# Kernel optimization log

Hardware: AMD Instinct MI355X
Metric: run time of the kernel (lower is better)

The kernel has to match this reference:

```python
import jax, jax.numpy as jnp
import numpy as np

SESSION_CHANNELS = [128, 160, 192, 224, 240, 248, 252, 256]  # per-session channel counts
N_SESS = len(SESSION_CHANNELS)
B, MAX_C, MAX_T = 16, 256, 4096
HID, N_SRC = 512, 256


def setup_inputs() -> dict:
    key = jax.random.key(0)
    ks = jax.random.split(key, 7)
    session_ids = jax.random.randint(ks[0], (B,), 0, N_SESS)
    chan_table = jnp.asarray(SESSION_CHANNELS)
    channel_counts = chan_table[session_ids]
    seq_lens = jax.random.randint(ks[1], (B,), MAX_T // 2, MAX_T + 1)
    x = jax.random.normal(ks[2], (B, MAX_C, MAX_T), jnp.float32)
    # zero-pad beyond true channels and true time (as the docstring states)
    cmask = (jnp.arange(MAX_C)[None, :] < channel_counts[:, None]).astype(x.dtype)
    tmask = (jnp.arange(MAX_T)[None, :] < seq_lens[:, None]).astype(x.dtype)
    x = x * cmask[:, :, None] * tmask[:, None, :]
    # per-session Linear(num_channels -> HID), padded to MAX_C rows (torch-style uniform init)
    lim1 = 1.0 / np.sqrt(MAX_C)
    W_sess = jax.random.uniform(ks[3], (N_SESS, MAX_C, HID), jnp.float32, -lim1, lim1)
    b_sess = jax.random.uniform(ks[4], (N_SESS, HID), jnp.float32, -lim1, lim1)
    lim2 = 1.0 / np.sqrt(HID)
    W2 = jax.random.uniform(ks[5], (HID, N_SRC), jnp.float32, -lim2, lim2)
    b2 = jax.random.uniform(ks[6], (N_SRC,), jnp.float32, -lim2, lim2)
    return dict(x=x, session_ids=session_ids, channel_counts=channel_counts,
                seq_lens=seq_lens, W_sess=W_sess, b_sess=b_sess, W2=W2, b2=b2)


def reference(x, session_ids, channel_counts, seq_lens, W_sess, b_sess, W2, b2):
    # mask padded channels so the full-width contraction equals the sliced per-sample matmul
    cmask = (jnp.arange(x.shape[1])[None, :] < channel_counts[:, None]).astype(x.dtype)
    xm = x * cmask[:, :, None]                       # (B, Max_C, Max_T)
    W = W_sess[session_ids]                          # (B, Max_C, HID) gathered per sample
    b = b_sess[session_ids]                          # (B, HID)
    h = jnp.einsum('bct,bch->bht', xm, W) + b[:, :, None]
    h = jax.nn.gelu(h, approximate=False)            # torch nn.GELU default is exact erf
    out = jnp.einsum('bht,hs->bst', h, W2) + b2[None, :, None]  # (B, N_SRC, Max_T)
    tmask = (jnp.arange(x.shape[2])[None, :] < seq_lens[:, None]).astype(x.dtype)
    return out * tmask[:, None, :]
```

## Files before the change

kernel.cpp:

```cpp
#include <hip/hip_runtime.h>

typedef __attribute__((ext_vector_type(8))) _Float16 f16x8;
typedef __attribute__((ext_vector_type(4))) _Float16 f16x4;
typedef __attribute__((ext_vector_type(2))) __fp16 fp16v2;
typedef __attribute__((ext_vector_type(4))) float f32x4;

#define NB 16
#define MAXC 256
#define MAXT 4096
#define HID 512
#define NSRC 256

#define BARV() asm volatile("s_waitcnt vmcnt(0) lgkmcnt(0)\n\ts_barrier" ::: "memory")
#define BAR() asm volatile("s_waitcnt lgkmcnt(0)\n\ts_barrier" ::: "memory")

#define MFMA(a, b, c) __builtin_amdgcn_mfma_f32_16x16x32_f16(a, b, c, 0, 0, 0)

typedef __attribute__((address_space(1))) const void gconst_void;
typedef __attribute__((address_space(3))) void lds_void;
#define GLOAD16(gp, lp) \
  __builtin_amdgcn_global_load_lds((gconst_void*)(gp), (lds_void*)(lp), 16, 0, 0)

__device__ __forceinline__ float gelu_fast(float x) {
  float p = x * x;
  float q = __builtin_fmaf(p, -0.10294336f, -2.30220778f);
  float e = __builtin_amdgcn_exp2f(x * q);
  return x * __builtin_amdgcn_rcpf(1.0f + e);
}

__device__ __forceinline__ void transpose_cvt_tile(const float* src, _Float16* dst,
                                                   int R, int C, int cx, int ry,
                                                   int tid) {
  __shared__ float tile[32][33];
  int c0 = cx * 32, r0 = ry * 32;
  int tx = tid & 31, ty = tid >> 5;
  for (int i = ty; i < 32; i += 8)
    tile[i][tx] = src[(size_t)(r0 + i) * C + (c0 + tx)];
  __syncthreads();
  for (int i = ty; i < 32; i += 8)
    dst[(size_t)(c0 + i) * R + (r0 + tx)] = (_Float16)tile[tx][i];
}

__global__ __launch_bounds__(256)
void prep_kernel(const float* __restrict__ x,
                 const int* __restrict__ seq_lens,
                 const int* __restrict__ chan_counts,
                 const float* __restrict__ W_sess,
                 const float* __restrict__ W2,
                 _Float16* __restrict__ xT,
                 _Float16* __restrict__ W1t,
                 _Float16* __restrict__ W2t) {
  int wg = blockIdx.x;
  int tid = threadIdx.x;

  if (wg >= 4096) {
    if (wg >= 5120) {
      int idx = wg - 5120;
      transpose_cvt_tile(W2, W2t, HID, NSRC, idx & 7, idx >> 3, tid);
    } else {
      int idx = wg - 4096;
      int z = idx >> 7;
      transpose_cvt_tile(W_sess + (size_t)z * MAXC * HID,
                         W1t + (size_t)z * MAXC * HID,
                         MAXC, HID, idx & 15, (idx >> 4) & 7, tid);
    }
    return;
  }

  int b = wg >> 8;
  int t0 = (wg & 63) * 64;
  int c0 = ((wg >> 6) & 3) * 64;
  int seqlen = seq_lens[b];
  if (t0 >= ((seqlen + 127) & ~127)) return;
  int wt = tid >> 5;
  int c2 = (tid & 31) * 2;
  _Float16* op = xT + ((size_t)b * MAXT + t0) * MAXC + c0;

  if (c0 >= chan_counts[b]) {
    #pragma unroll
    for (int i = 0; i < 8; ++i) {
      fp16v2 z = {(_Float16)0.f, (_Float16)0.f};
      *(fp16v2*)(op + (size_t)(wt + i * 8) * MAXC + c2) = z;
    }
    return;
  }

  __shared__ float tile[64][65];
  int tx = tid & 63, ty = tid >> 6;
  const float* xp = x + ((size_t)b * MAXC + c0) * MAXT + t0;
  #pragma unroll
  for (int i = 0; i < 16; ++i) {
    int c = ty + i * 4;
    tile[c][tx] = xp[(size_t)c * MAXT + tx];
  }
  __syncthreads();
  #pragma unroll
  for (int i = 0; i < 8; ++i) {
    int tl = wt + i * 8;
    fp16v2 p = __builtin_amdgcn_cvt_pkrtz(tile[c2][tl], tile[c2 + 1][tl]);
    *(fp16v2*)(op + (size_t)tl * MAXC + c2) = p;
  }
}


__global__ __launch_bounds__(512, 2)
void gemm1_kernel(const _Float16* __restrict__ xT,
                  const int* __restrict__ sess_ids,
                  const int* __restrict__ seq_lens,
                  const _Float16* __restrict__ W1t,
                  const float* __restrict__ b_sess,
                  _Float16* __restrict__ h_t) {
  int wg = blockIdx.x;
  int nt = wg & 31;
  int mt = (wg >> 5) & 1;
  int b = wg >> 6;
  int tb0 = nt * 128, h0 = mt * 256;
  int seqlen = seq_lens[b];
  if (tb0 >= seqlen) return;
  int sid = sess_ids[b];

  __shared__ _Float16 As[256 * 64];
  __shared__ _Float16 Bs[128 * 64];

  int tid = threadIdx.x;
  int lane = tid & 63, w = tid >> 6;
  int wr = w >> 1, wc = w & 1;
  int lg = lane >> 4, lr = lane & 15;

  f32x4 acc[4][4];
  #pragma unroll
  for (int mi = 0; mi < 4; ++mi) {
    f32x4 bv = *(const f32x4*)(b_sess + sid * HID + h0 + wr * 64 + mi * 16 + lg * 4);
    #pragma unroll
    for (int ni = 0; ni < 4; ++ni) acc[mi][ni] = bv;
  }

  int rsub = lane >> 3;
  int swb = ((lane & 7) ^ rsub) * 16;
  const char* gA = (const char*)(W1t + (size_t)sid * HID * MAXC + (size_t)h0 * MAXC)
                   + (size_t)(w * 32 + rsub) * 512 + swb;
  const char* gB = (const char*)(xT + ((size_t)b * MAXT + tb0) * MAXC)
                   + (size_t)(w * 16 + rsub) * 512 + swb;
  char* lA = (char*)As + w * 4096;
  char* lB = (char*)Bs + w * 2048;

#define STAGE1(kc)                                                        \
  {                                                                       \
    _Pragma("unroll")                                                     \
    for (int j = 0; j < 4; ++j)                                           \
      GLOAD16(gA + (size_t)(kc)*128 + (size_t)j * 8 * 512, lA + j * 1024); \
    _Pragma("unroll")                                                     \
    for (int j = 0; j < 2; ++j)                                           \
      GLOAD16(gB + (size_t)(kc)*128 + (size_t)j * 8 * 512, lB + j * 1024); \
  }

  STAGE1(0);
  BARV();

  #pragma unroll 1
  for (int kc = 0; kc < 4; ++kc) {
    #pragma unroll
    for (int slot = 0; slot < 2; ++slot) {
      f16x8 af[4], bf[4];
      #pragma unroll
      for (int mi = 0; mi < 4; ++mi) {
        int row = wr * 64 + mi * 16 + lr;
        af[mi] = *(const f16x8*)(&As[row * 64 + (((slot * 4 + lg) ^ (row & 7)) * 8)]);
      }
      #pragma unroll
      for (int ni = 0; ni < 4; ++ni) {
        int t = wc * 64 + ni * 16 + lr;
        bf[ni] = *(const f16x8*)(&Bs[t * 64 + (((slot * 4 + lg) ^ (t & 7)) * 8)]);
      }
      __builtin_amdgcn_s_setprio(1);
      #pragma unroll
      for (int mi = 0; mi < 4; ++mi)
        #pragma unroll
        for (int ni = 0; ni < 4; ++ni)
          acc[mi][ni] = MFMA(af[mi], bf[ni], acc[mi][ni]);
      __builtin_amdgcn_s_setprio(0);
    }
    if (kc < 3) {
      BAR();
      STAGE1(kc + 1);
      BARV();
    }
  }

  _Float16* hp = h_t + (size_t)b * MAXT * HID;
  #pragma unroll
  for (int mi = 0; mi < 4; ++mi) {
    int h = h0 + wr * 64 + mi * 16 + lg * 4;
    #pragma unroll
    for (int ni = 0; ni < 4; ++ni) {
      int t = tb0 + wc * 64 + ni * 16 + lr;
      f16x4 g;
      #pragma unroll
      for (int r = 0; r < 4; ++r) g[r] = (_Float16)gelu_fast(acc[mi][ni][r]);
      *(f16x4*)(hp + (size_t)t * HID + h) = g;
    }
  }
}

__global__ __launch_bounds__(512, 2)
void gemm2_kernel(const int* __restrict__ seq_lens,
                  const _Float16* __restrict__ W2t,
                  const float* __restrict__ b2,
                  const _Float16* __restrict__ h_t,
                  float* __restrict__ out) {
  int wg = blockIdx.x;
  int nt = wg & 31;
  int b = wg >> 5;
  int tb0 = nt * 128;
  int seqlen = seq_lens[b];
  int tid = threadIdx.x;

  if (tb0 >= seqlen) {
    int sr = tid >> 1, tq = (tid & 1) * 64;
    float* po = out + ((size_t)b * NSRC + sr) * MAXT + tb0 + tq;
    f32x4 z = {0.f, 0.f, 0.f, 0.f};
    #pragma unroll
    for (int i = 0; i < 16; ++i) *(f32x4*)(po + i * 4) = z;
    return;
  }

  __shared__ _Float16 As[256 * 64];
  __shared__ _Float16 Bs[128 * 64];

  int lane = tid & 63, w = tid >> 6;
  int wr = w >> 1, wc = w & 1;
  int lg = lane >> 4, lr = lane & 15;

  f32x4 acc[4][4];
  #pragma unroll
  for (int mi = 0; mi < 4; ++mi) {
    f32x4 bv = *(const f32x4*)(b2 + wr * 64 + mi * 16 + lg * 4);
    #pragma unroll
    for (int ni = 0; ni < 4; ++ni) acc[mi][ni] = bv;
  }

  int rsub = lane >> 3;
  int swb = ((lane & 7) ^ rsub) * 16;
  const char* gA = (const char*)W2t + (size_t)(w * 32 + rsub) * 1024 + swb;
  const char* gB = (const char*)(h_t + ((size_t)b * MAXT + tb0) * HID)
                   + (size_t)(w * 16 + rsub) * 1024 + swb;
  char* lA = (char*)As + w * 4096;
  char* lB = (char*)Bs + w * 2048;

#define STAGE2(kc)                                                         \
  {                                                                        \
    _Pragma("unroll")                                                      \
    for (int j = 0; j < 4; ++j)                                            \
      GLOAD16(gA + (size_t)(kc)*128 + (size_t)j * 8 * 1024, lA + j * 1024); \
    _Pragma("unroll")                                                      \
    for (int j = 0; j < 2; ++j)                                            \
      GLOAD16(gB + (size_t)(kc)*128 + (size_t)j * 8 * 1024, lB + j * 1024); \
  }

  STAGE2(0);
  BARV();

  #pragma unroll 1
  for (int kc = 0; kc < 8; ++kc) {
    #pragma unroll
    for (int slot = 0; slot < 2; ++slot) {
      f16x8 af[4], bf[4];
      #pragma unroll
      for (int mi = 0; mi < 4; ++mi) {
        int row = wr * 64 + mi * 16 + lr;
        af[mi] = *(const f16x8*)(&As[row * 64 + (((slot * 4 + lg) ^ (row & 7)) * 8)]);
      }
      #pragma unroll
      for (int ni = 0; ni < 4; ++ni) {
        int t = wc * 64 + ni * 16 + lr;
        bf[ni] = *(const f16x8*)(&Bs[t * 64 + (((slot * 4 + lg) ^ (t & 7)) * 8)]);
      }
      __builtin_amdgcn_s_setprio(1);
      #pragma unroll
      for (int mi = 0; mi < 4; ++mi)
        #pragma unroll
        for (int ni = 0; ni < 4; ++ni)
          acc[mi][ni] = MFMA(af[mi], bf[ni], acc[mi][ni]);
      __builtin_amdgcn_s_setprio(0);
    }
    if (kc < 7) {
      BAR();
      STAGE2(kc + 1);
      BARV();
    }
  }

  #pragma unroll
  for (int mi = 0; mi < 4; ++mi) {
    int s = wr * 64 + mi * 16 + lg * 4;
    #pragma unroll
    for (int ni = 0; ni < 4; ++ni) {
      int t = tb0 + wc * 64 + ni * 16 + lr;
      float m = (t < seqlen) ? 1.0f : 0.0f;
      #pragma unroll
      for (int r = 0; r < 4; ++r)
        out[((size_t)b * NSRC + s + r) * MAXT + t] = acc[mi][ni][r] * m;
    }
  }
}

extern "C" void kernel_launch(void* const* d_in, const int* in_sizes, int n_in,
                              void* d_out, int out_size, void* d_ws, size_t ws_size,
                              hipStream_t stream) {
  const float* x      = (const float*)d_in[0];
  const int* sess     = (const int*)d_in[1];
  const int* ccnt     = (const int*)d_in[2];
  const int* seq      = (const int*)d_in[3];
  const float* W_sess = (const float*)d_in[4];
  const float* b_sess = (const float*)d_in[5];
  const float* W2     = (const float*)d_in[6];
  const float* b2     = (const float*)d_in[7];
  float* out = (float*)d_out;

  char* wp = (char*)d_ws;
  _Float16* W1t = (_Float16*)wp;                     wp += (size_t)8 * HID * MAXC * 2;
  _Float16* W2t = (_Float16*)wp;                     wp += (size_t)NSRC * HID * 2;
  _Float16* h_t = (_Float16*)wp;                     wp += (size_t)NB * MAXT * HID * 2;
  _Float16* xT  = (_Float16*)wp;

  prep_kernel<<<dim3(4096 + 1024 + 128), dim3(256), 0, stream>>>(
      x, seq, ccnt, W_sess, W2, xT, W1t, W2t);
  gemm1_kernel<<<dim3(NB * 2 * 32), dim3(512), 0, stream>>>(xT, sess, seq, W1t, b_sess, h_t);
  gemm2_kernel<<<dim3(NB * 32), dim3(512), 0, stream>>>(seq, W2t, b2, h_t, out);
}
```

Measured before the change: 77.14 us.

## Double-buffer activation tiles and remap block order across XCDs in both GEMMs

Both GEMM kernels now double-buffer the B (activation) tile in LDS and issue the next chunk's B load before computing the current chunk, so that load overlaps the MFMA work. The A (weight) tile still loads after the barrier. Block IDs are also remapped so consecutive workgroups on the same XCD (pid&7) cover neighbouring tiles of the same batch, which is meant to improve L2 reuse of the weights and activations. LDS use rises by 16KB per block, which could lower occupancy at 2 blocks per CU.

```diff
diff --git a/kernel.cpp b/kernel.cpp
--- a/kernel.cpp
+++ b/kernel.cpp
@@ -110,17 +110,18 @@
                   const _Float16* __restrict__ W1t,
                   const float* __restrict__ b_sess,
                   _Float16* __restrict__ h_t) {
-  int wg = blockIdx.x;
-  int nt = wg & 31;
-  int mt = (wg >> 5) & 1;
-  int b = wg >> 6;
+  int pid = blockIdx.x;
+  int L = (pid & 7) * 128 + (pid >> 3);
+  int mt = L & 1;
+  int nt = (L >> 1) & 31;
+  int b = L >> 6;
   int tb0 = nt * 128, h0 = mt * 256;
   int seqlen = seq_lens[b];
   if (tb0 >= seqlen) return;
   int sid = sess_ids[b];
 
   __shared__ _Float16 As[256 * 64];
-  __shared__ _Float16 Bs[128 * 64];
+  __shared__ _Float16 Bs[2][128 * 64];
 
   int tid = threadIdx.x;
   int lane = tid & 63, w = tid >> 6;
@@ -142,23 +143,25 @@
   const char* gB = (const char*)(xT + ((size_t)b * MAXT + tb0) * MAXC)
                    + (size_t)(w * 16 + rsub) * 512 + swb;
   char* lA = (char*)As + w * 4096;
-  char* lB = (char*)Bs + w * 2048;
-
-#define STAGE1(kc)                                                        \
-  {                                                                       \
-    _Pragma("unroll")                                                     \
-    for (int j = 0; j < 4; ++j)                                           \
-      GLOAD16(gA + (size_t)(kc)*128 + (size_t)j * 8 * 512, lA + j * 1024); \
-    _Pragma("unroll")                                                     \
-    for (int j = 0; j < 2; ++j)                                           \
-      GLOAD16(gB + (size_t)(kc)*128 + (size_t)j * 8 * 512, lB + j * 1024); \
-  }
-
-  STAGE1(0);
+
+#define STAGE1_A(kc)                                                      \
+  _Pragma("unroll")                                                       \
+  for (int j = 0; j < 4; ++j)                                             \
+    GLOAD16(gA + (size_t)(kc)*128 + (size_t)j * 8 * 512, lA + j * 1024);
+#define STAGE1_B(kc, bb)                                                  \
+  _Pragma("unroll")                                                       \
+  for (int j = 0; j < 2; ++j)                                             \
+    GLOAD16(gB + (size_t)(kc)*128 + (size_t)j * 8 * 512,                  \
+            (char*)Bs[bb] + w * 2048 + j * 1024);
+
+  STAGE1_A(0);
+  STAGE1_B(0, 0);
   BARV();
 
   #pragma unroll 1
   for (int kc = 0; kc < 4; ++kc) {
+    int cur = kc & 1;
+    if (kc < 3) STAGE1_B(kc + 1, cur ^ 1);
     #pragma unroll
     for (int slot = 0; slot < 2; ++slot) {
       f16x8 af[4], bf[4];
@@ -170,7 +173,7 @@
       #pragma unroll
       for (int ni = 0; ni < 4; ++ni) {
         int t = wc * 64 + ni * 16 + lr;
-        bf[ni] = *(const f16x8*)(&Bs[t * 64 + (((slot * 4 + lg) ^ (t & 7)) * 8)]);
+        bf[ni] = *(const f16x8*)(&Bs[cur][t * 64 + (((slot * 4 + lg) ^ (t & 7)) * 8)]);
       }
       __builtin_amdgcn_s_setprio(1);
       #pragma unroll
@@ -182,7 +185,7 @@
     }
     if (kc < 3) {
       BAR();
-      STAGE1(kc + 1);
+      STAGE1_A(kc + 1);
       BARV();
     }
   }
@@ -208,9 +211,10 @@
                   const float* __restrict__ b2,
                   const _Float16* __restrict__ h_t,
                   float* __restrict__ out) {
-  int wg = blockIdx.x;
-  int nt = wg & 31;
-  int b = wg >> 5;
+  int pid = blockIdx.x;
+  int L = (pid & 7) * 64 + (pid >> 3);
+  int nt = L & 31;
+  int b = L >> 5;
   int tb0 = nt * 128;
   int seqlen = seq_lens[b];
   int tid = threadIdx.x;
@@ -225,7 +229,7 @@
   }
 
   __shared__ _Float16 As[256 * 64];
-  __shared__ _Float16 Bs[128 * 64];
+  __shared__ _Float16 Bs[2][128 * 64];
 
   int lane = tid & 63, w = tid >> 6;
   int wr = w >> 1, wc = w & 1;
@@ -245,23 +249,25 @@
   const char* gB = (const char*)(h_t + ((size_t)b * MAXT + tb0) * HID)
                    + (size_t)(w * 16 + rsub) * 1024 + swb;
   char* lA = (char*)As + w * 4096;
-  char* lB = (char*)Bs + w * 2048;
-
-#define STAGE2(kc)                                                         \
-  {                                                                        \
-    _Pragma("unroll")                                                      \
-    for (int j = 0; j < 4; ++j)                                            \
-      GLOAD16(gA + (size_t)(kc)*128 + (size_t)j * 8 * 1024, lA + j * 1024); \
-    _Pragma("unroll")                                                      \
-    for (int j = 0; j < 2; ++j)                                            \
-      GLOAD16(gB + (size_t)(kc)*128 + (size_t)j * 8 * 1024, lB + j * 1024); \
-  }
-
-  STAGE2(0);
+
+#define STAGE2_A(kc)                                                       \
+  _Pragma("unroll")                                                        \
+  for (int j = 0; j < 4; ++j)                                              \
+    GLOAD16(gA + (size_t)(kc)*128 + (size_t)j * 8 * 1024, lA + j * 1024);
+#define STAGE2_B(kc, bb)                                                   \
+  _Pragma("unroll")                                                        \
+  for (int j = 0; j < 2; ++j)                                              \
+    GLOAD16(gB + (size_t)(kc)*128 + (size_t)j * 8 * 1024,                  \
+            (char*)Bs[bb] + w * 2048 + j * 1024);
+
+  STAGE2_A(0);
+  STAGE2_B(0, 0);
   BARV();
 
   #pragma unroll 1
   for (int kc = 0; kc < 8; ++kc) {
+    int cur = kc & 1;
+    if (kc < 7) STAGE2_B(kc + 1, cur ^ 1);
     #pragma unroll
     for (int slot = 0; slot < 2; ++slot) {
       f16x8 af[4], bf[4];
@@ -273,7 +279,7 @@
       #pragma unroll
       for (int ni = 0; ni < 4; ++ni) {
         int t = wc * 64 + ni * 16 + lr;
-        bf[ni] = *(const f16x8*)(&Bs[t * 64 + (((slot * 4 + lg) ^ (t & 7)) * 8)]);
+        bf[ni] = *(const f16x8*)(&Bs[cur][t * 64 + (((slot * 4 + lg) ^ (t & 7)) * 8)]);
       }
       __builtin_amdgcn_s_setprio(1);
       #pragma unroll
@@ -285,7 +291,7 @@
     }
     if (kc < 7) {
       BAR();
-      STAGE2(kc + 1);
+      STAGE2_A(kc + 1);
       BARV();
     }
   }
```

Result: no change. 76.84 us (-0.4%).
